# Optimization experiments

Hardware: AMD Instinct MI355X
Metric: run time of the kernel (lower is better)

The kernel has to match this reference:

```python
import jax, jax.numpy as jnp
import numpy as np

EPS = 1e-8  # numerical guard in padded (masked) softmax denominator


def setup_inputs() -> dict:
    key = jax.random.key(0)
    k1, k2 = jax.random.split(key)
    B, N, D = 8, 2048, 3
    coordinates = jax.random.normal(k1, (B, N, D), dtype=jnp.float32)
    masks = (jax.random.uniform(k2, (B, N, N)) < 0.9).astype(jnp.float32)
    sigma = jnp.ones((1,), dtype=jnp.float32)  # NonNeg learned scalar
    return {"coordinates": coordinates, "masks": masks, "sigma": sigma}


def reference(coordinates, masks, sigma):
    # pairwise squared euclidean distances: ||xi||^2 - 2 xi.xj + ||xj||^2
    norms = jnp.sum(coordinates ** 2, axis=-1, keepdims=True)            # [B,N,1]
    inner = jnp.einsum('bnd,bmd->bnm', coordinates, coordinates)         # [B,N,N]
    distances = norms - 2.0 * inner + jnp.swapaxes(norms, -1, -2)        # [B,N,N]
    # Gaussian kernel
    A = jnp.exp(-distances / (sigma ** 2))                               # [B,N,N]
    # padded_softmax: mask then row-normalize (A is positive, so this is a
    # masked softmax over -d/sigma^2 along the last axis)
    A = A * masks
    return A / (jnp.sum(A, axis=-1, keepdims=True) + EPS)
```

## Files before the change

kernel.cpp:

```cpp
#include <hip/hip_runtime.h>
#include <math.h>


#define NN 2048
#define THREADS 256
#define EPS 1e-8f

__global__ __launch_bounds__(THREADS) void gauss_adj_kernel(
    const float* __restrict__ coords,
    const float* __restrict__ masks,
    const float* __restrict__ sigma,
    float* __restrict__ out)
{
    const int row = blockIdx.x;
    const int b   = row >> 11;
    const int i   = row & (NN - 1);
    const int tid = threadIdx.x;

    __shared__ __align__(16) float sx[NN];
    __shared__ __align__(16) float sy[NN];
    __shared__ __align__(16) float sz[NN];
    __shared__ float red[THREADS / 64];
    __shared__ float s_inv;

    const float* cb = coords + (size_t)b * NN * 3;
    for (int idx = tid; idx < NN; idx += THREADS) {
        sx[idx] = cb[idx * 3 + 0];
        sy[idx] = cb[idx * 3 + 1];
        sz[idx] = cb[idx * 3 + 2];
    }
    __syncthreads();

    const float xi = sx[i];
    const float yi = sy[i];
    const float zi = sz[i];
    const float s  = sigma[0];
    const float inv_s2 = 1.0f / (s * s);

    const float4* mrow = (const float4*)(masks + (size_t)row * NN);
    float4*       orow = (float4*)(out + (size_t)row * NN);
    const float4* sx4 = (const float4*)sx;
    const float4* sy4 = (const float4*)sy;
    const float4* sz4 = (const float4*)sz;

    float vals[8];
    float lsum = 0.0f;

    #pragma unroll
    for (int c = 0; c < 2; ++c) {
        const int j4 = c * THREADS + tid;
        const float4 m = mrow[j4];
        const float4 X = sx4[j4];
        const float4 Y = sy4[j4];
        const float4 Z = sz4[j4];
        const float mx[4] = {m.x, m.y, m.z, m.w};
        const float xs[4] = {X.x, X.y, X.z, X.w};
        const float ys[4] = {Y.x, Y.y, Y.z, Y.w};
        const float zs[4] = {Z.x, Z.y, Z.z, Z.w};
        #pragma unroll
        for (int k = 0; k < 4; ++k) {
            const float dx = xi - xs[k];
            const float dy = yi - ys[k];
            const float dz = zi - zs[k];
            const float d  = dx * dx + dy * dy + dz * dz;
            const float a  = __expf(-d * inv_s2) * mx[k];
            vals[c * 4 + k] = a;
            lsum += a;
        }
    }

    #pragma unroll
    for (int off = 32; off > 0; off >>= 1)
        lsum += __shfl_down(lsum, off, 64);
    const int wave = tid >> 6;
    if ((tid & 63) == 0) red[wave] = lsum;
    __syncthreads();
    if (tid == 0) {
        float tot = red[0] + red[1] + red[2] + red[3];
        s_inv = 1.0f / (tot + EPS);
    }
    __syncthreads();
    const float inv = s_inv;

    #pragma unroll
    for (int c = 0; c < 2; ++c) {
        const int j4 = c * THREADS + tid;
        float4 o;
        o.x = vals[c * 4 + 0] * inv;
        o.y = vals[c * 4 + 1] * inv;
        o.z = vals[c * 4 + 2] * inv;
        o.w = vals[c * 4 + 3] * inv;
        orow[j4] = o;
    }
}

extern "C" void kernel_launch(void* const* d_in, const int* in_sizes, int n_in,
                              void* d_out, int out_size, void* d_ws, size_t ws_size,
                              hipStream_t stream) {
    const float* coords = (const float*)d_in[0];
    const float* masks  = (const float*)d_in[1];
    const float* sigma  = (const float*)d_in[2];
    float* out = (float*)d_out;

    const int B = in_sizes[0] / (NN * 3);
    const int rows = B * NN;
    gauss_adj_kernel<<<rows, THREADS, 0, stream>>>(coords, masks, sigma, out);
}
```

Measured before the change: 232.7 us.

## Process one row per wavefront, drop shared-memory staging, use nontemporal loads/stores

Each 64-lane wavefront now handles one full row instead of a 256-thread block per row, so the row-sum reduction is a pure wave shuffle with no __syncthreads or LDS. The per-block staging of all coordinates into shared memory is removed; coordinates are read directly from global memory (L2/L1-cached) as packed float4 triples. Mask loads and output stores use nontemporal hints to avoid polluting caches with streaming data. This raises registers per thread (32 floats held) and relies on cache hits for the repeated coordinate reads.

```diff
diff --git a/kernel.cpp b/kernel.cpp
--- a/kernel.cpp
+++ b/kernel.cpp
@@ -2,9 +2,12 @@
 #include <math.h>
 
 
-#define NN 2048
+#define NN      2048
 #define THREADS 256
-#define EPS 1e-8f
+#define WPB     4
+#define EPS     1e-8f
+
+typedef float vfloat4 __attribute__((ext_vector_type(4)));
 
 __global__ __launch_bounds__(THREADS) void gauss_adj_kernel(
     const float* __restrict__ coords,
@@ -12,85 +15,68 @@
     const float* __restrict__ sigma,
     float* __restrict__ out)
 {
-    const int row = blockIdx.x;
-    const int b   = row >> 11;
-    const int i   = row & (NN - 1);
-    const int tid = threadIdx.x;
-
-    __shared__ __align__(16) float sx[NN];
-    __shared__ __align__(16) float sy[NN];
-    __shared__ __align__(16) float sz[NN];
-    __shared__ float red[THREADS / 64];
-    __shared__ float s_inv;
+    const int row  = blockIdx.x * WPB + (threadIdx.x >> 6);
+    const int lane = threadIdx.x & 63;
+    const int b    = row >> 11;
+    const int i    = row & (NN - 1);
 
     const float* cb = coords + (size_t)b * NN * 3;
-    for (int idx = tid; idx < NN; idx += THREADS) {
-        sx[idx] = cb[idx * 3 + 0];
-        sy[idx] = cb[idx * 3 + 1];
-        sz[idx] = cb[idx * 3 + 2];
-    }
-    __syncthreads();
-
-    const float xi = sx[i];
-    const float yi = sy[i];
-    const float zi = sz[i];
+    const float xi = cb[i * 3 + 0];
+    const float yi = cb[i * 3 + 1];
+    const float zi = cb[i * 3 + 2];
     const float s  = sigma[0];
     const float inv_s2 = 1.0f / (s * s);
 
-    const float4* mrow = (const float4*)(masks + (size_t)row * NN);
-    float4*       orow = (float4*)(out + (size_t)row * NN);
-    const float4* sx4 = (const float4*)sx;
-    const float4* sy4 = (const float4*)sy;
-    const float4* sz4 = (const float4*)sz;
+    const vfloat4* mrow = (const vfloat4*)(masks + (size_t)row * NN);
+    vfloat4*       orow = (vfloat4*)(out + (size_t)row * NN);
+    const float4*  c4   = (const float4*)cb;
 
-    float vals[8];
+    vfloat4 a[8];
     float lsum = 0.0f;
 
     #pragma unroll
-    for (int c = 0; c < 2; ++c) {
-        const int j4 = c * THREADS + tid;
-        const float4 m = mrow[j4];
-        const float4 X = sx4[j4];
-        const float4 Y = sy4[j4];
-        const float4 Z = sz4[j4];
-        const float mx[4] = {m.x, m.y, m.z, m.w};
-        const float xs[4] = {X.x, X.y, X.z, X.w};
-        const float ys[4] = {Y.x, Y.y, Y.z, Y.w};
-        const float zs[4] = {Z.x, Z.y, Z.z, Z.w};
-        #pragma unroll
-        for (int k = 0; k < 4; ++k) {
-            const float dx = xi - xs[k];
-            const float dy = yi - ys[k];
-            const float dz = zi - zs[k];
-            const float d  = dx * dx + dy * dy + dz * dz;
-            const float a  = __expf(-d * inv_s2) * mx[k];
-            vals[c * 4 + k] = a;
-            lsum += a;
-        }
+    for (int w = 0; w < 8; ++w) {
+        const int q = w * 64 + lane;
+        const vfloat4 m = __builtin_nontemporal_load(&mrow[q]);
+        const float4 c0 = c4[3 * q + 0];
+        const float4 c1 = c4[3 * q + 1];
+        const float4 c2 = c4[3 * q + 2];
+
+        float dx, dy, dz, d;
+        dx = xi - c0.x; dy = yi - c0.y; dz = zi - c0.z;
+        d  = dx * dx + dy * dy + dz * dz;
+        const float a0 = __expf(-d * inv_s2) * m.x;
+
+        dx = xi - c0.w; dy = yi - c1.x; dz = zi - c1.y;
+        d  = dx * dx + dy * dy + dz * dz;
+        const float a1 = __expf(-d * inv_s2) * m.y;
+
+        dx = xi - c1.z; dy = yi - c1.w; dz = zi - c2.x;
+        d  = dx * dx + dy * dy + dz * dz;
+        const float a2 = __expf(-d * inv_s2) * m.z;
+
+        dx = xi - c2.y; dy = yi - c2.z; dz = zi - c2.w;
+        d  = dx * dx + dy * dy + dz * dz;
+        const float a3 = __expf(-d * inv_s2) * m.w;
+
+        vfloat4 av;
+        av.x = a0; av.y = a1; av.z = a2; av.w = a3;
+        a[w] = av;
+        lsum += (a0 + a1) + (a2 + a3);
     }
 
     #pragma unroll
     for (int off = 32; off > 0; off >>= 1)
-        lsum += __shfl_down(lsum, off, 64);
-    const int wave = tid >> 6;
-    if ((tid & 63) == 0) red[wave] = lsum;
-    __syncthreads();
-    if (tid == 0) {
-        float tot = red[0] + red[1] + red[2] + red[3];
-        s_inv = 1.0f / (tot + EPS);
-    }
-    __syncthreads();
-    const float inv = s_inv;
+        lsum += __shfl_xor(lsum, off, 64);
+
+    const float inv = 1.0f / (lsum + EPS);
 
     #pragma unroll
-    for (int c = 0; c < 2; ++c) {
-        const int j4 = c * THREADS + tid;
-        float4 o;
-        o.x = vals[c * 4 + 0] * inv;
-        o.y = vals[c * 4 + 1] * inv;
-        o.z = vals[c * 4 + 2] * inv;
-        o.w = vals[c * 4 + 3] * inv;
-        orow[j4] = o;
+    for (int w = 0; w < 8; ++w) {
+        const int q = w * 64 + lane;
+        vfloat4 o = a[w];
+        o.x *= inv; o.y *= inv; o.z *= inv; o.w *= inv;
+        __builtin_nontemporal_store(o, &orow[q]);
     }
 }
 
@@ -102,7 +88,7 @@
     const float* sigma  = (const float*)d_in[2];
     float* out = (float*)d_out;
 
-    const int B = in_sizes[0] / (NN * 3);
+    const int B    = in_sizes[0] / (NN * 3);
     const int rows = B * NN;
-    gauss_adj_kernel<<<rows, THREADS, 0, stream>>>(coords, masks, sigma, out);
+    gauss_adj_kernel<<<rows / WPB, THREADS, 0, stream>>>(coords, masks, sigma, out);
 }
```

Result: no change. 237.2 us (+1.9%).
